# Kernel optimization log

Measured on AMD Instinct MI355X. Metric: run time of the kernel, lower is better.

## Reference

```python
import jax, jax.numpy as jnp
import numpy as np

T = 2048
N = 4096
DT = 0.01
V_RESET = 1.0
ALPHA = 0.01
MAX_SPIKES = 128


def setup_inputs() -> dict:
    key = jax.random.key(0)
    ks = jax.random.split(key, 8)
    ts = jnp.arange(T, dtype=jnp.float32) * DT
    input_current = jax.random.normal(ks[0], (T, N), dtype=jnp.float32)
    # _build_w: uniform(minval=0.5) fully-connected weight matrix
    w = jax.random.uniform(ks[1], (N, N), dtype=jnp.float32, minval=0.5, maxval=1.0)
    # _build_initial: uniform(maxval=0.1)
    v0 = jax.random.uniform(ks[2], (N,), dtype=jnp.float32, maxval=0.1)
    i0 = jax.random.uniform(ks[3], (N,), dtype=jnp.float32, maxval=0.1)
    mu = jax.random.uniform(ks[4], (2,), dtype=jnp.float32, minval=0.5, maxval=1.0)
    # uniforms for initial s and for post-spike s resampling (s = log(u) - alpha)
    s0_u = jax.random.uniform(ks[5], (N,), dtype=jnp.float32)
    resample_u = jax.random.uniform(ks[6], (T, N), dtype=jnp.float32)
    return {"ts": ts, "input_current": input_current, "w": w, "v0": v0,
            "i0": i0, "mu": mu, "s0_u": s0_u, "resample_u": resample_u,
            "max_spikes": MAX_SPIKES}


def reference(ts, input_current, w, v0, i0, mu, s0_u, resample_u, max_spikes):
    """Event-driven spiking net: Euler integration of the drift vf with
    spike events when s crosses 0, followed by the masked per-neuron jump
    transition (_inner_trans_fn) using the firing neuron's weight row.
    Returns trajectory ys [T, N, 3] (v, i, s per neuron)."""
    dt = ts[1] - ts[0]
    eps = jnp.float32(1e-12)
    # s0 = log(uniform) - alpha  (always negative; drifts up at rate intensity(v))
    s0 = jnp.log(s0_u + eps) - ALPHA
    y0 = jnp.stack([v0, i0, s0], axis=-1)  # [N, 3]
    mu1, mu2 = mu[0], mu[1]

    def step(carry, xs):
        y, nsp = carry
        inp_t, ru_t = xs
        v, i, s = y[:, 0], y[:, 1], y[:, 2]
        # drift_vf (Euler step)
        v_n = v + dt * (mu1 * (i - v) + mu1 * inp_t)
        i_n = i + dt * (-mu2 * i)
        s_n = s + dt * jax.nn.sigmoid(v)  # intensity_fn(v)
        # event detection: cond_fn = s; event when s reaches 0
        ev = s_n >= 0.0  # [N] event mask
        fire = jnp.any(ev) & (nsp < max_spikes)
        idx = jnp.argmax(ev)  # event_idx = argmax over event mask
        w_row = w[idx]  # weights from firing neuron to all neurons
        # _inner_trans_fn: spiking neurons reset v and resample s;
        # non-spiking neurons receive current injection w[idx][j]
        v_t = jnp.where(ev, v_n - V_RESET, v_n)
        i_t = jnp.where(ev, i_n, i_n + w_row)
        s_t = jnp.where(ev, jnp.log(ru_t + eps) - ALPHA, s_n)
        y_fire = jnp.stack([v_t, i_t, s_t], axis=-1)
        y_free = jnp.stack([v_n, i_n, s_n], axis=-1)
        y_out = jnp.where(fire, y_fire, y_free)
        nsp = nsp + fire.astype(jnp.int32)
        return (y_out, nsp), y_out

    (_, _), ys = jax.lax.scan(step, (y0, jnp.int32(0)),
                              (input_current, resample_u))
    return ys
```

## Files before the change

kernel.cpp:

```cpp
#include <hip/hip_runtime.h>
#include <stddef.h>

#define TT 2048
#define NN 4096
#define LSEG 64
#define NSEG (TT / LSEG)
#define NBLK 16
#define TPA 64
#define NPT 4
#define TPB 256
#define MAXU 0xFFFFFFFFu
#define NOFIRE 0xFFFFFFFEu

__global__ __launch_bounds__(TPA) void phaseA(
    const float* __restrict__ ts, const float* __restrict__ inp,
    const float* __restrict__ w, const float* __restrict__ v0,
    const float* __restrict__ i0, const float* __restrict__ mu,
    const float* __restrict__ s0u, const float* __restrict__ ru,
    const int* __restrict__ mx, float* __restrict__ ys,
    unsigned int* __restrict__ hdr, unsigned int* __restrict__ slots)
{
#pragma clang fp contract(off)
  const int tid = threadIdx.x;
  const int blk = blockIdx.x;
  const int idx4 = blk * TPA + tid;
  const int n0 = idx4 * NPT;
  const float dt = ts[1] - ts[0];
  const float mu1 = mu[0], mu2 = mu[1];
  const int maxs = mx[0];

  const float4* inp4 = (const float4*)inp;
  const float4* ru4  = (const float4*)ru;
  const float4* w4   = (const float4*)w;

  float4 a4;
  a4 = ((const float4*)v0)[idx4];  float v[NPT]    = {a4.x, a4.y, a4.z, a4.w};
  a4 = ((const float4*)i0)[idx4];  float i_nw[NPT] = {a4.x, a4.y, a4.z, a4.w};
  a4 = ((const float4*)s0u)[idx4];
  float s[NPT] = {logf(a4.x + 1e-12f) - 0.01f, logf(a4.y + 1e-12f) - 0.01f,
                  logf(a4.z + 1e-12f) - 0.01f, logf(a4.w + 1e-12f) - 0.01f};

  float snP[NPT] = {0.f, 0.f, 0.f, 0.f};
  bool  evP[NPT] = {false, false, false, false};
  bool  aw[NPT]  = {false, false, false, false};
  float wvP[NPT] = {0.f, 0.f, 0.f, 0.f};
  float4 inp_prev = make_float4(0.f,0.f,0.f,0.f);
  float4 ru_prev  = make_float4(0.f,0.f,0.f,0.f);
  int nsp = 0;
  int t_stop = TT;
  bool pubbed = false;

  for (int t = 0; t <= TT; ++t) {
    unsigned int gm1 = NOFIRE;
    if (t >= 1 && pubbed) {
      const unsigned int* row = &slots[(size_t)(t - 1) * NBLK];
      unsigned int x = MAXU;
      long g = 0;
      for (;;) {
        x = __hip_atomic_load(&row[tid & (NBLK - 1)], __ATOMIC_RELAXED,
                              __HIP_MEMORY_SCOPE_AGENT);
        if (__ballot(x != MAXU) == ~0ULL) break;
        if (++g > (1L << 20)) break;
      }
      gm1 = x;
#pragma unroll
      for (int off = 1; off < NBLK; off <<= 1) {
        unsigned int o = (unsigned int)__shfl_xor((int)gm1, off, 64);
        gm1 = gm1 < o ? gm1 : o;
      }
    }
    bool fire1 = (gm1 < (unsigned int)NN) && (nsp < maxs);
    if (fire1) nsp += 1;

    float4 inp_pref = make_float4(0.f,0.f,0.f,0.f);
    float4 ru_pref  = make_float4(0.f,0.f,0.f,0.f);
    if (t < TT) {
      inp_pref = inp4[(size_t)t * (NN / 4) + idx4];
      ru_pref  = ru4[(size_t)t * (NN / 4) + idx4];
    }
    float4 wrN = make_float4(0.f,0.f,0.f,0.f);
    if (fire1) wrN = w4[(size_t)gm1 * (NN / 4) + idx4];

    if (t >= 1) {
      float ifull[NPT];
#pragma unroll
      for (int k = 0; k < NPT; ++k) ifull[k] = aw[k] ? (i_nw[k] + wvP[k]) : i_nw[k];
      if (t >= 2) {
        size_t o = ((size_t)(t - 2) * NN + (size_t)n0) * 3;
        float4* yo = (float4*)(ys + o);
        yo[0] = make_float4(v[0], ifull[0], s[0], v[1]);
        yo[1] = make_float4(ifull[1], s[1], v[2], ifull[2]);
        yo[2] = make_float4(s[2], v[3], ifull[3], s[3]);
      }
      float iv[NPT] = {inp_prev.x, inp_prev.y, inp_prev.z, inp_prev.w};
      float rv[NPT] = {ru_prev.x,  ru_prev.y,  ru_prev.z,  ru_prev.w};
      float vn[NPT], in_[NPT];
#pragma unroll
      for (int k = 0; k < NPT; ++k) {
        vn[k]  = v[k] + dt * (mu1 * (ifull[k] - v[k]) + mu1 * iv[k]);
        in_[k] = ifull[k] + dt * (-mu2 * ifull[k]);
      }
      if (fire1) {
#pragma unroll
        for (int k = 0; k < NPT; ++k) {
          if (evP[k]) {
            v[k] = vn[k] - 1.0f;
            s[k] = logf(rv[k] + 1e-12f) - 0.01f;
            aw[k] = false;
          } else {
            v[k] = vn[k]; s[k] = snP[k]; aw[k] = true;
          }
        }
      } else {
#pragma unroll
        for (int k = 0; k < NPT; ++k) { v[k] = vn[k]; s[k] = snP[k]; aw[k] = false; }
      }
#pragma unroll
      for (int k = 0; k < NPT; ++k) i_nw[k] = in_[k];
      wvP[0] = wrN.x; wvP[1] = wrN.y; wvP[2] = wrN.z; wvP[3] = wrN.w;
      if (t == TT || (nsp >= maxs && (t & (LSEG - 1)) == 0)) { t_stop = t; break; }
    }

    {
      unsigned int m = NOFIRE;
#pragma unroll
      for (int k = 0; k < NPT; ++k) {
        float sig = 1.0f / (1.0f + expf(-v[k]));
        float sn = s[k] + dt * sig;
        bool e = sn >= 0.0f;
        snP[k] = sn; evP[k] = e;
        unsigned int c = e ? (unsigned int)(n0 + k) : NOFIRE;
        m = m < c ? m : c;
      }
      if (nsp < maxs) {
#pragma unroll
        for (int off = 1; off < 64; off <<= 1) {
          unsigned int o = (unsigned int)__shfl_xor((int)m, off, 64);
          m = m < o ? m : o;
        }
        if (tid == 0)
          __hip_atomic_store(&slots[(size_t)t * NBLK + blk], m,
                             __ATOMIC_RELAXED, __HIP_MEMORY_SCOPE_AGENT);
        pubbed = true;
      } else {
        pubbed = false;
      }
    }
    inp_prev = inp_pref; ru_prev = ru_pref;
  }

  {
    float ifull[NPT];
#pragma unroll
    for (int k = 0; k < NPT; ++k) ifull[k] = aw[k] ? (i_nw[k] + wvP[k]) : i_nw[k];
    size_t o = ((size_t)(t_stop - 1) * NN + (size_t)n0) * 3;
    float4* yo = (float4*)(ys + o);
    yo[0] = make_float4(v[0], ifull[0], s[0], v[1]);
    yo[1] = make_float4(ifull[1], s[1], v[2], ifull[2]);
    yo[2] = make_float4(s[2], v[3], ifull[3], s[3]);
  }
  if (blk == 0 && tid == 0) hdr[0] = (unsigned int)t_stop;
}

__global__ __launch_bounds__(TPB) void p1_segc(
    const float* __restrict__ ts, const float* __restrict__ inp,
    const float* __restrict__ mu, const float* __restrict__ ys,
    const unsigned int* __restrict__ hdr, float* __restrict__ buf1)
{
  unsigned int Kp = hdr[0];
  unsigned int g0 = Kp / LSEG;
  unsigned int g = blockIdx.x >> 4;
  if (g < g0) return;
  int n = (blockIdx.x & 15) * TPB + threadIdx.x;
  float dt = ts[1] - ts[0];
  float mu1 = mu[0], mu2 = mu[1];
  float a = 1.0f - dt * mu1, b = dt * mu1, r = 1.0f - dt * mu2;
  float ibase = ys[((size_t)(Kp - 1) * NN + n) * 3 + 1];
  float ij = ibase * powf(r, (float)((int)(g * LSEG) - (int)Kp));
  float c = 0.0f;
  size_t base = (size_t)(g * LSEG) * NN + n;
  for (int j = 0; j < LSEG; ++j) {
    float x = inp[base + (size_t)j * NN];
    c = a * c + b * (ij + x);
    ij *= r;
  }
  buf1[(size_t)g * NN + n] = c;
}

__global__ __launch_bounds__(TPB) void p2_scanv(
    const float* __restrict__ ts, const float* __restrict__ mu,
    const float* __restrict__ ys, const unsigned int* __restrict__ hdr,
    float* __restrict__ buf1)
{
  unsigned int Kp = hdr[0];
  unsigned int g0 = Kp / LSEG;
  if (g0 >= NSEG) return;
  int n = blockIdx.x * TPB + threadIdx.x;
  float dt = ts[1] - ts[0];
  float mu1 = mu[0];
  float a = 1.0f - dt * mu1;
  float aL = a;
  for (int k = 0; k < 6; ++k) aL *= aL;
  float v = ys[((size_t)(Kp - 1) * NN + n) * 3 + 0];
  for (unsigned int g = g0; g < NSEG; ++g) {
    float cg = buf1[(size_t)g * NN + n];
    buf1[(size_t)g * NN + n] = v;
    v = aL * v + cg;
  }
}

__global__ __launch_bounds__(TPB) void p3_seg(
    const float* __restrict__ ts, const float* __restrict__ inp,
    const float* __restrict__ mu, const unsigned int* __restrict__ hdr,
    const float* __restrict__ buf1, float* __restrict__ buf2,
    float* __restrict__ ys)
{
  unsigned int Kp = hdr[0];
  unsigned int g0 = Kp / LSEG;
  unsigned int g = blockIdx.x >> 4;
  if (g < g0) return;
  int n = (blockIdx.x & 15) * TPB + threadIdx.x;
  float dt = ts[1] - ts[0];
  float mu1 = mu[0], mu2 = mu[1];
  float r = 1.0f - dt * mu2;
  float v = buf1[(size_t)g * NN + n];
  float ibase = ys[((size_t)(Kp - 1) * NN + n) * 3 + 1];
  float i = ibase * powf(r, (float)((int)(g * LSEG) - (int)Kp));
  float sl = 0.0f;
  for (int j = 0; j < LSEG; ++j) {
    size_t t = (size_t)g * LSEG + j;
    float x = inp[t * NN + n];
    float sig = 1.0f / (1.0f + expf(-v));
    sl = sl + dt * sig;
    float vn  = v + dt * (mu1 * (i - v) + mu1 * x);
    float in_ = i + dt * (-mu2 * i);
    size_t o = (t * NN + n) * 3;
    ys[o] = vn; ys[o + 1] = in_; ys[o + 2] = sl;
    v = vn; i = in_;
  }
  buf2[(size_t)g * NN + n] = sl;
}

__global__ __launch_bounds__(TPB) void p4_scans(
    const float* __restrict__ ys, const unsigned int* __restrict__ hdr,
    float* __restrict__ buf2)
{
  unsigned int Kp = hdr[0];
  unsigned int g0 = Kp / LSEG;
  if (g0 >= NSEG) return;
  int n = blockIdx.x * TPB + threadIdx.x;
  float s = ys[((size_t)(Kp - 1) * NN + n) * 3 + 2];
  for (unsigned int g = g0; g < NSEG; ++g) {
    float t = buf2[(size_t)g * NN + n];
    buf2[(size_t)g * NN + n] = s;
    s += t;
  }
}

__global__ __launch_bounds__(TPB) void p5_fixs(
    const unsigned int* __restrict__ hdr, const float* __restrict__ buf2,
    float* __restrict__ ys)
{
  unsigned int Kp = hdr[0];
  size_t e = (size_t)Kp * NN + (size_t)blockIdx.x * TPB + threadIdx.x;
  if (e >= (size_t)TT * NN) return;
  unsigned int t = (unsigned int)(e >> 12);
  unsigned int n = (unsigned int)(e & (NN - 1));
  unsigned int g = t >> 6;
  ys[e * 3 + 2] += buf2[(size_t)g * NN + n];
}

extern "C" void kernel_launch(void* const* d_in, const int* in_sizes, int n_in,
                              void* d_out, int out_size, void* d_ws, size_t ws_size,
                              hipStream_t stream)
{
  (void)in_sizes; (void)n_in; (void)out_size; (void)ws_size;
  const float* ts  = (const float*)d_in[0];
  const float* inp = (const float*)d_in[1];
  const float* w   = (const float*)d_in[2];
  const float* v0  = (const float*)d_in[3];
  const float* i0  = (const float*)d_in[4];
  const float* mu  = (const float*)d_in[5];
  const float* s0u = (const float*)d_in[6];
  const float* ru  = (const float*)d_in[7];
  const int*   mx  = (const int*)d_in[8];
  float* ys = (float*)d_out;

  char* wsb = (char*)d_ws;
  unsigned int* hdr   = (unsigned int*)wsb;
  unsigned int* slots = (unsigned int*)(wsb + 1024);
  float* buf1 = (float*)(wsb + 1024 + (size_t)TT * NBLK * 4);
  float* buf2 = buf1 + (size_t)NSEG * NN;

  hipMemsetAsync(slots, 0xFF, (size_t)TT * NBLK * 4, stream);

  phaseA<<<NBLK, TPA, 0, stream>>>(ts, inp, w, v0, i0, mu, s0u, ru, mx, ys, hdr, slots);
  p1_segc<<<NSEG * 16, TPB, 0, stream>>>(ts, inp, mu, ys, hdr, buf1);
  p2_scanv<<<NN / TPB, TPB, 0, stream>>>(ts, mu, ys, hdr, buf1);
  p3_seg<<<NSEG * 16, TPB, 0, stream>>>(ts, inp, mu, hdr, buf1, buf2, ys);
  p4_scans<<<NN / TPB, TPB, 0, stream>>>(ys, hdr, buf2);
  p5_fixs<<<(TT - 128) * NN / TPB, TPB, 0, stream>>>(hdr, buf2, ys);
}
```

Before: 647.1 us.

## Split serial spike phase into event-discovery kernel and parallel trajectory replay

The sequential 16-block spike-detection kernel no longer writes the trajectory. It only records the firing times and indices, and it pipelines the cross-block reduction two steps deep so the spin-wait overlaps with local compute. A second kernel with 64 blocks replays the dynamics per neuron from the recorded spike list, with weights staged in LDS, and writes ys in parallel. This is meant to take global stores and w-row loads off the latency-bound serial loop, at the cost of an extra kernel launch and a recomputed prefix. The stop time is now rounded up to the next segment boundary, which changes how the work is split with the later scan kernels.

```diff
diff --git a/kernel.cpp b/kernel.cpp
--- a/kernel.cpp
+++ b/kernel.cpp
@@ -9,16 +9,18 @@
 #define TPA 64
 #define NPT 4
 #define TPB 256
+#define WCAP 256
 #define MAXU 0xFFFFFFFFu
 #define NOFIRE 0xFFFFFFFEu
 
-__global__ __launch_bounds__(TPA) void phaseA(
+__global__ __launch_bounds__(TPA) void phaseA1(
     const float* __restrict__ ts, const float* __restrict__ inp,
     const float* __restrict__ w, const float* __restrict__ v0,
     const float* __restrict__ i0, const float* __restrict__ mu,
     const float* __restrict__ s0u, const float* __restrict__ ru,
-    const int* __restrict__ mx, float* __restrict__ ys,
-    unsigned int* __restrict__ hdr, unsigned int* __restrict__ slots)
+    const int* __restrict__ mx, unsigned int* __restrict__ hdr,
+    unsigned int* __restrict__ slots, unsigned int* __restrict__ fireT,
+    unsigned int* __restrict__ fireIdx)
 {
 #pragma clang fp contract(off)
   const int tid = threadIdx.x;
@@ -44,122 +46,191 @@
   bool  evP[NPT] = {false, false, false, false};
   bool  aw[NPT]  = {false, false, false, false};
   float wvP[NPT] = {0.f, 0.f, 0.f, 0.f};
-  float4 inp_prev = make_float4(0.f,0.f,0.f,0.f);
-  float4 ru_prev  = make_float4(0.f,0.f,0.f,0.f);
+  float4 inp_cur = make_float4(0.f,0.f,0.f,0.f);
+  float4 ru_cur  = make_float4(0.f,0.f,0.f,0.f);
   int nsp = 0;
   int t_stop = TT;
-  bool pubbed = false;
-
-  for (int t = 0; t <= TT; ++t) {
-    unsigned int gm1 = NOFIRE;
-    if (t >= 1 && pubbed) {
-      const unsigned int* row = &slots[(size_t)(t - 1) * NBLK];
-      unsigned int x = MAXU;
-      long g = 0;
-      for (;;) {
-        x = __hip_atomic_load(&row[tid & (NBLK - 1)], __ATOMIC_RELAXED,
-                              __HIP_MEMORY_SCOPE_AGENT);
-        if (__ballot(x != MAXU) == ~0ULL) break;
-        if (++g > (1L << 20)) break;
-      }
-      gm1 = x;
-#pragma unroll
-      for (int off = 1; off < NBLK; off <<= 1) {
-        unsigned int o = (unsigned int)__shfl_xor((int)gm1, off, 64);
-        gm1 = gm1 < o ? gm1 : o;
-      }
-    }
-    bool fire1 = (gm1 < (unsigned int)NN) && (nsp < maxs);
-    if (fire1) nsp += 1;
-
-    float4 inp_pref = make_float4(0.f,0.f,0.f,0.f);
-    float4 ru_pref  = make_float4(0.f,0.f,0.f,0.f);
-    if (t < TT) {
-      inp_pref = inp4[(size_t)t * (NN / 4) + idx4];
-      ru_pref  = ru4[(size_t)t * (NN / 4) + idx4];
-    }
-    float4 wrN = make_float4(0.f,0.f,0.f,0.f);
-    if (fire1) wrN = w4[(size_t)gm1 * (NN / 4) + idx4];
-
+  bool pubPrev = false;
+
+  for (int t = 0;; ++t) {
+    bool  fire2 = false;
+    bool  awN[NPT] = {false, false, false, false};
+    float wN[NPT]  = {0.f, 0.f, 0.f, 0.f};
+
+    if (t >= 2) {
+      unsigned int gm2 = NOFIRE;
+      if (pubPrev) {
+        const unsigned int* row = &slots[(size_t)(t - 2) * NBLK];
+        unsigned int x = MAXU;
+        long g = 0;
+        for (;;) {
+          x = __hip_atomic_load(&row[tid & (NBLK - 1)], __ATOMIC_RELAXED,
+                                __HIP_MEMORY_SCOPE_AGENT);
+          if (__ballot(x != MAXU) == ~0ULL) break;
+          if (++g > (1L << 20)) break;
+        }
+        gm2 = x;
+#pragma unroll
+        for (int off = 1; off < NBLK; off <<= 1) {
+          unsigned int o = (unsigned int)__shfl_xor((int)gm2, off, 64);
+          gm2 = gm2 < o ? gm2 : o;
+        }
+      }
+      fire2 = (gm2 < (unsigned int)NN) && (nsp < maxs);
+      if (fire2) {
+        if (blk == 0 && tid == 0 && nsp < WCAP) {
+          fireT[nsp] = (unsigned int)(t - 2);
+          fireIdx[nsp] = gm2;
+        }
+        float4 wr = w4[(size_t)gm2 * (NN / 4) + idx4];
+        wN[0] = wr.x; wN[1] = wr.y; wN[2] = wr.z; wN[3] = wr.w;
+#pragma unroll
+        for (int k = 0; k < NPT; ++k) awN[k] = !evP[k];
+        nsp += 1;
+        if (nsp >= maxs) {
+          t_stop = ((t - 1 + LSEG - 1) / LSEG) * LSEG;
+          if (t_stop > TT) t_stop = TT;
+          break;
+        }
+      }
+      if (t - 1 == TT) { t_stop = TT; break; }
+    }
+
+    if (t >= 2) {
+      float iv[NPT] = {inp_cur.x, inp_cur.y, inp_cur.z, inp_cur.w};
+      float rv[NPT] = {ru_cur.x,  ru_cur.y,  ru_cur.z,  ru_cur.w};
+#pragma unroll
+      for (int k = 0; k < NPT; ++k) {
+        float ifull = aw[k] ? (i_nw[k] + wvP[k]) : i_nw[k];
+        float vn  = v[k] + dt * (mu1 * (ifull - v[k]) + mu1 * iv[k]);
+        float in_ = ifull + dt * (-mu2 * ifull);
+        if (evP[k] && fire2) {
+          v[k] = vn - 1.0f;
+          s[k] = logf(rv[k] + 1e-12f) - 0.01f;
+        } else {
+          v[k] = vn; s[k] = snP[k];
+        }
+        i_nw[k] = in_;
+      }
+    }
+
+    bool pubNow = false;
+    bool evN[NPT] = {false, false, false, false};
     if (t >= 1) {
-      float ifull[NPT];
-#pragma unroll
-      for (int k = 0; k < NPT; ++k) ifull[k] = aw[k] ? (i_nw[k] + wvP[k]) : i_nw[k];
-      if (t >= 2) {
-        size_t o = ((size_t)(t - 2) * NN + (size_t)n0) * 3;
-        float4* yo = (float4*)(ys + o);
-        yo[0] = make_float4(v[0], ifull[0], s[0], v[1]);
-        yo[1] = make_float4(ifull[1], s[1], v[2], ifull[2]);
-        yo[2] = make_float4(s[2], v[3], ifull[3], s[3]);
-      }
-      float iv[NPT] = {inp_prev.x, inp_prev.y, inp_prev.z, inp_prev.w};
-      float rv[NPT] = {ru_prev.x,  ru_prev.y,  ru_prev.z,  ru_prev.w};
-      float vn[NPT], in_[NPT];
-#pragma unroll
-      for (int k = 0; k < NPT; ++k) {
-        vn[k]  = v[k] + dt * (mu1 * (ifull[k] - v[k]) + mu1 * iv[k]);
-        in_[k] = ifull[k] + dt * (-mu2 * ifull[k]);
-      }
-      if (fire1) {
-#pragma unroll
-        for (int k = 0; k < NPT; ++k) {
-          if (evP[k]) {
-            v[k] = vn[k] - 1.0f;
-            s[k] = logf(rv[k] + 1e-12f) - 0.01f;
-            aw[k] = false;
-          } else {
-            v[k] = vn[k]; s[k] = snP[k]; aw[k] = true;
-          }
-        }
-      } else {
-#pragma unroll
-        for (int k = 0; k < NPT; ++k) { v[k] = vn[k]; s[k] = snP[k]; aw[k] = false; }
-      }
-#pragma unroll
-      for (int k = 0; k < NPT; ++k) i_nw[k] = in_[k];
-      wvP[0] = wrN.x; wvP[1] = wrN.y; wvP[2] = wrN.z; wvP[3] = wrN.w;
-      if (t == TT || (nsp >= maxs && (t & (LSEG - 1)) == 0)) { t_stop = t; break; }
-    }
-
-    {
       unsigned int m = NOFIRE;
 #pragma unroll
       for (int k = 0; k < NPT; ++k) {
         float sig = 1.0f / (1.0f + expf(-v[k]));
         float sn = s[k] + dt * sig;
+        snP[k] = sn;
         bool e = sn >= 0.0f;
-        snP[k] = sn; evP[k] = e;
+        evN[k] = e;
         unsigned int c = e ? (unsigned int)(n0 + k) : NOFIRE;
         m = m < c ? m : c;
       }
-      if (nsp < maxs) {
-#pragma unroll
-        for (int off = 1; off < 64; off <<= 1) {
-          unsigned int o = (unsigned int)__shfl_xor((int)m, off, 64);
-          m = m < o ? m : o;
-        }
-        if (tid == 0)
-          __hip_atomic_store(&slots[(size_t)t * NBLK + blk], m,
-                             __ATOMIC_RELAXED, __HIP_MEMORY_SCOPE_AGENT);
-        pubbed = true;
-      } else {
-        pubbed = false;
-      }
-    }
-    inp_prev = inp_pref; ru_prev = ru_pref;
-  }
-
-  {
-    float ifull[NPT];
-#pragma unroll
-    for (int k = 0; k < NPT; ++k) ifull[k] = aw[k] ? (i_nw[k] + wvP[k]) : i_nw[k];
-    size_t o = ((size_t)(t_stop - 1) * NN + (size_t)n0) * 3;
-    float4* yo = (float4*)(ys + o);
-    yo[0] = make_float4(v[0], ifull[0], s[0], v[1]);
-    yo[1] = make_float4(ifull[1], s[1], v[2], ifull[2]);
-    yo[2] = make_float4(s[2], v[3], ifull[3], s[3]);
-  }
-  if (blk == 0 && tid == 0) hdr[0] = (unsigned int)t_stop;
+#pragma unroll
+      for (int off = 1; off < 64; off <<= 1) {
+        unsigned int o = (unsigned int)__shfl_xor((int)m, off, 64);
+        m = m < o ? m : o;
+      }
+      if (tid == 0)
+        __hip_atomic_store(&slots[(size_t)(t - 1) * NBLK + blk], m,
+                           __ATOMIC_RELAXED, __HIP_MEMORY_SCOPE_AGENT);
+      pubNow = true;
+    }
+
+    float4 inw = make_float4(0.f,0.f,0.f,0.f);
+    float4 rnw = make_float4(0.f,0.f,0.f,0.f);
+    if (t >= 1 && t - 1 < TT) {
+      inw = inp4[(size_t)(t - 1) * (NN / 4) + idx4];
+      rnw = ru4[(size_t)(t - 1) * (NN / 4) + idx4];
+    }
+
+#pragma unroll
+    for (int k = 0; k < NPT; ++k) {
+      evP[k] = evN[k]; aw[k] = awN[k]; wvP[k] = wN[k];
+    }
+    inp_cur = inw; ru_cur = rnw;
+    pubPrev = pubNow;
+  }
+
+  if (blk == 0 && tid == 0) {
+    hdr[0] = (unsigned int)t_stop;
+    hdr[1] = (unsigned int)nsp;
+  }
+}
+
+__global__ __launch_bounds__(TPA) void phaseA2(
+    const float* __restrict__ ts, const float* __restrict__ inp,
+    const float* __restrict__ w, const float* __restrict__ v0,
+    const float* __restrict__ i0, const float* __restrict__ mu,
+    const float* __restrict__ s0u, const float* __restrict__ ru,
+    const unsigned int* __restrict__ hdr, const unsigned int* __restrict__ fireT,
+    const unsigned int* __restrict__ fireIdx, float* __restrict__ ys)
+{
+#pragma clang fp contract(off)
+  const int tid = threadIdx.x;
+  const int n = blockIdx.x * TPA + tid;
+  const int Kp = (int)hdr[0];
+  int nf = (int)hdr[1]; if (nf > WCAP) nf = WCAP;
+  const float dt = ts[1] - ts[0];
+  const float mu1 = mu[0], mu2 = mu[1];
+
+  __shared__ unsigned int sT[WCAP];
+  __shared__ float wlds[WCAP][TPA];
+  for (int k = tid; k < nf; k += TPA) sT[k] = fireT[k];
+  for (int k0 = 0; k0 < nf; k0 += 8) {
+    float tmp[8];
+#pragma unroll
+    for (int j = 0; j < 8; ++j) {
+      int k = k0 + j;
+      tmp[j] = (k < nf) ? w[(size_t)fireIdx[k] * NN + n] : 0.0f;
+    }
+#pragma unroll
+    for (int j = 0; j < 8; ++j) {
+      int k = k0 + j;
+      if (k < nf) wlds[k][tid] = tmp[j];
+    }
+  }
+  __syncthreads();
+
+  float v = v0[n];
+  float i = i0[n];
+  float s = logf(s0u[n] + 1e-12f) - 0.01f;
+
+  float ib[8], rb[8];
+#pragma unroll
+  for (int j = 0; j < 8; ++j) {
+    ib[j] = inp[(size_t)j * NN + n];
+    rb[j] = ru[(size_t)j * NN + n];
+  }
+  int kp = 0;
+  for (int tb = 0; tb < Kp; tb += 8) {
+#pragma unroll
+    for (int j = 0; j < 8; ++j) {
+      const int t = tb + j;
+      const float x   = ib[j];
+      const float ruv = rb[j];
+      if (t + 8 < Kp) {
+        ib[j] = inp[(size_t)(t + 8) * NN + n];
+        rb[j] = ru[(size_t)(t + 8) * NN + n];
+      }
+      float sig = 1.0f / (1.0f + expf(-v));
+      float sn = s + dt * sig;
+      bool e = sn >= 0.0f;
+      float vn  = v + dt * (mu1 * (i - v) + mu1 * x);
+      float in_ = i + dt * (-mu2 * i);
+      bool fire = (kp < nf) && (sT[kp] == (unsigned int)t);
+      if (fire) {
+        float wc = wlds[kp][tid];
+        ++kp;
+        if (e) { v = vn - 1.0f; i = in_;      s = logf(ruv + 1e-12f) - 0.01f; }
+        else   { v = vn;        i = in_ + wc; s = sn; }
+      } else   { v = vn;        i = in_;      s = sn; }
+      size_t o = ((size_t)t * NN + n) * 3;
+      *(float3*)(ys + o) = make_float3(v, i, s);
+    }
+  }
 }
 
 __global__ __launch_bounds__(TPB) void p1_segc(
@@ -287,14 +358,19 @@
   float* ys = (float*)d_out;
 
   char* wsb = (char*)d_ws;
-  unsigned int* hdr   = (unsigned int*)wsb;
-  unsigned int* slots = (unsigned int*)(wsb + 1024);
-  float* buf1 = (float*)(wsb + 1024 + (size_t)TT * NBLK * 4);
+  unsigned int* hdr     = (unsigned int*)wsb;
+  unsigned int* fireT   = (unsigned int*)(wsb + 256);
+  unsigned int* fireIdx = (unsigned int*)(wsb + 1280);
+  unsigned int* slots   = (unsigned int*)(wsb + 4096);
+  float* buf1 = (float*)(wsb + 4096 + (size_t)TT * NBLK * 4);
   float* buf2 = buf1 + (size_t)NSEG * NN;
 
   hipMemsetAsync(slots, 0xFF, (size_t)TT * NBLK * 4, stream);
 
-  phaseA<<<NBLK, TPA, 0, stream>>>(ts, inp, w, v0, i0, mu, s0u, ru, mx, ys, hdr, slots);
+  phaseA1<<<NBLK, TPA, 0, stream>>>(ts, inp, w, v0, i0, mu, s0u, ru, mx,
+                                    hdr, slots, fireT, fireIdx);
+  phaseA2<<<NN / TPA, TPA, 0, stream>>>(ts, inp, w, v0, i0, mu, s0u, ru,
+                                        hdr, fireT, fireIdx, ys);
   p1_segc<<<NSEG * 16, TPB, 0, stream>>>(ts, inp, mu, ys, hdr, buf1);
   p2_scanv<<<NN / TPB, TPB, 0, stream>>>(ts, mu, ys, hdr, buf1);
   p3_seg<<<NSEG * 16, TPB, 0, stream>>>(ts, inp, mu, hdr, buf1, buf2, ys);
```

New measurement: 654.9 us. Within noise of the previous version (+1.2%).
